# Kernel tuning notes

Measured on AMD Instinct MI355X. Metric: run time of the kernel, lower is better.

Reference implementation:

```python
import jax, jax.numpy as jnp
import numpy as np

EPS_LN = 1e-12
EPS_BN = 1e-5


def layernorm(x, w, b):
    u = jnp.mean(x, axis=-1, keepdims=True)
    s = jnp.mean((x - u) ** 2, axis=-1, keepdims=True)
    return w * ((x - u) / jnp.sqrt(s + EPS_LN)) + b


def reps_block(x, ln1_w, ln1_b, lin_w, lin_b, ln2_w, ln2_b):
    # GRAPHLayerNorm -> (dropout, identity in eval) -> Linear -> ReLU -> GRAPHLayerNorm
    h = layernorm(x, ln1_w, ln1_b)
    h = jax.nn.relu(jnp.einsum('bnd,od->bno', h, lin_w) + lin_b)
    return layernorm(h, ln2_w, ln2_b)


def attend(x):
    # full dense self-attention: softmax(x x^T) x ; dropout is identity in eval
    scores = jnp.einsum('bnd,bmd->bnm', x, x)  # [B,4096,4096]
    attn = jax.nn.softmax(scores, axis=-1)
    return jnp.einsum('bnm,bmd->bnd', attn, x)


def setup_inputs() -> dict:
    key = jax.random.key(0)
    ks = jax.random.split(key, 8)
    B, C, H, W = 4, 512, 64, 64
    D = 512
    inp = {
        'T1': jax.random.normal(ks[0], (B, C, H, W), jnp.float32),
        'T2': jax.random.normal(ks[1], (B, C, H, W), jnp.float32),
        'w_conv3': jax.random.normal(ks[2], (1024, 1024, 3, 3), jnp.float32) * 0.01,
        'w_conv1': jax.random.normal(ks[3], (512, 1024, 1, 1), jnp.float32) * 0.03,
        'bn_gamma': jnp.ones((512,), jnp.float32),
        'bn_beta': jnp.zeros((512,), jnp.float32),
        'bn_mean': jnp.zeros((512,), jnp.float32),
        'bn_var': jnp.ones((512,), jnp.float32),
        'ln1_w': jnp.ones((D,), jnp.float32),
        'ln1_b': jnp.zeros((D,), jnp.float32),
        'lin_w': jax.random.normal(ks[4], (D, D), jnp.float32) * 0.04,
        'lin_b': jnp.zeros((D,), jnp.float32),
        'ln2_w': jnp.ones((D,), jnp.float32),
        'ln2_b': jnp.zeros((D,), jnp.float32),
    }
    return inp


def reference(T1, T2, w_conv3, w_conv1, bn_gamma, bn_beta, bn_mean, bn_var,
              ln1_w, ln1_b, lin_w, lin_b, ln2_w, ln2_b):
    B = T1.shape[0]
    X = jnp.concatenate((T1, T2), axis=1)  # [B,1024,64,64]
    dn = ('NCHW', 'OIHW', 'NCHW')
    X = jax.lax.conv_general_dilated(X, w_conv3, (1, 1), ((1, 1), (1, 1)), dimension_numbers=dn)
    X = jax.lax.conv_general_dilated(X, w_conv1, (1, 1), ((0, 0), (0, 0)), dimension_numbers=dn)  # [B,512,64,64]
    # BatchNorm (eval, running stats) + ReLU
    inv = (bn_gamma / jnp.sqrt(bn_var + EPS_BN))[None, :, None, None]
    X = jax.nn.relu(X * inv + (bn_beta - bn_mean * bn_gamma / jnp.sqrt(bn_var + EPS_BN))[None, :, None, None])
    x = X.transpose(0, 2, 3, 1).reshape(B, 4096, 512)
    # block 1
    rel = attend(x)
    rel = reps_block(x + rel, ln1_w, ln1_b, lin_w, lin_b, ln2_w, ln2_b)
    # block 2 (original code reuses self.reps_graph, i.e. SAME params)
    rel1 = attend(rel)
    rel1 = reps_block(rel + rel1, ln1_w, ln1_b, lin_w, lin_b, ln2_w, ln2_b)
    return rel1.reshape(B, 64, 64, 512).transpose(0, 3, 1, 2)  # [B,512,64,64]
```

## Files before the change

### kernel.cpp

```cpp
#include <hip/hip_runtime.h>
#include <stdint.h>

typedef float f32x4 __attribute__((ext_vector_type(4)));
typedef __bf16 bf16x8 __attribute__((ext_vector_type(8)));
typedef unsigned short u16;
typedef unsigned short u16x8 __attribute__((ext_vector_type(8)));

__device__ __forceinline__ float bf2f(u16 u){ unsigned int i = ((unsigned int)u)<<16; float f; __builtin_memcpy(&f,&i,4); return f; }
__device__ __forceinline__ u16 f2bf(float f){ unsigned int i; __builtin_memcpy(&i,&f,4); i += 0x7FFFu + ((i>>16)&1u); return (u16)(i>>16); }
__device__ __forceinline__ u16 f2h(float f){ _Float16 h = (_Float16)f; u16 b; __builtin_memcpy(&b,&h,2); return b; }
__device__ __forceinline__ float h2f(u16 b){ _Float16 h; __builtin_memcpy(&h,&b,2); return (float)h; }

__device__ __forceinline__ void gld16(const void* g, void* l){
  __builtin_amdgcn_global_load_lds(
      (const __attribute__((address_space(1))) void*)(uintptr_t)g,
      (__attribute__((address_space(3))) void*)(unsigned int)(uintptr_t)l, 16, 0, 0);
}

__global__ __launch_bounds__(256) void pad_interior(const float* __restrict__ T1,
                                                    const float* __restrict__ T2,
                                                    u16* __restrict__ Xpad){
  const int n = blockIdx.z, ct = blockIdx.y, pt = blockIdx.x;
  const int t = threadIdx.x;
  const int c0 = ct*64, p0 = pt*64;
  const float* src = (c0 < 512) ? (T1 + ((long)n*512 + c0)*4096)
                                : (T2 + ((long)n*512 + (c0-512))*4096);
  __shared__ u16 lds[64][66];
  #pragma unroll
  for (int i=0;i<4;i++){
    int c = i*16 + (t>>4);
    int ch = t&15;
    float4 v = *(const float4*)(src + (long)c*4096 + p0 + ch*4);
    int p = ch*4;
    lds[p+0][c] = f2bf(v.x); lds[p+1][c] = f2bf(v.y);
    lds[p+2][c] = f2bf(v.z); lds[p+3][c] = f2bf(v.w);
  }
  __syncthreads();
  #pragma unroll
  for (int i=0;i<8;i++){
    int p = i*8 + (t>>5);
    int c2 = t&31;
    int pix = p0 + p; int yy = (pix>>6)+1, xx = (pix&63)+1;
    ushort2 val; val.x = lds[p][2*c2]; val.y = lds[p][2*c2+1];
    *(ushort2*)(Xpad + (((long)n*66 + yy)*66 + xx)*1024 + c0 + 2*c2) = val;
  }
}

__global__ __launch_bounds__(256) void prep_w3(const float* __restrict__ w3, u16* __restrict__ wk3t){
  const int o = blockIdx.x; const int t = threadIdx.x;
  __shared__ u16 lds[9216];
  const float* src = w3 + (long)o*9216;
  #pragma unroll
  for (int i=0;i<9;i++){
    int j = i*256 + t;
    float4 v = *(const float4*)(src + j*4);
    lds[j*4+0]=f2bf(v.x); lds[j*4+1]=f2bf(v.y); lds[j*4+2]=f2bf(v.z); lds[j*4+3]=f2bf(v.w);
  }
  __syncthreads();
  u16* dst = wk3t + (long)o*9216;
  #pragma unroll
  for (int i=0;i<36;i++){
    int j = i*256 + t; int tp = j>>10, ci = j&1023;
    dst[j] = lds[ci*9+tp];
  }
}

__global__ void prep_small(const float* __restrict__ w1, const float* __restrict__ bg,
                           const float* __restrict__ bb, const float* __restrict__ bm,
                           const float* __restrict__ bv, const float* __restrict__ linw,
                           u16* __restrict__ w1t, u16* __restrict__ lint,
                           float* __restrict__ bias1){
  const int b = blockIdx.x, t = threadIdx.x;
  if (b < 2048){
    long i = (long)b*256 + t;
    int o = (int)(i>>10);
    float inv = bg[o] / sqrtf(bv[o] + 1e-5f);
    w1t[i] = f2bf(w1[i]*inv);
  } else if (b < 3072){
    long i = (long)(b-2048)*256 + t;
    lint[i] = f2bf(linw[i]);
  } else {
    int o = (b-3072)*256 + t;
    float inv = bg[o]/sqrtf(bv[o]+1e-5f);
    bias1[o] = bb[o] - bm[o]*inv;
  }
}

__global__ __launch_bounds__(256) void row_norm(const u16* __restrict__ x, float* __restrict__ nrm){
  const int row = blockIdx.x*4 + (threadIdx.x>>6);
  const int lane = threadIdx.x & 63;
  u16x8 q = *(const u16x8*)(x + (long)row*512 + lane*8);
  float s = 0.f;
  #pragma unroll
  for (int j=0;j<8;j++){ float f = bf2f(q[j]); s += f*f; }
  #pragma unroll
  for (int off=32; off; off>>=1) s += __shfl_xor(s, off);
  if (lane==0) nrm[row] = s;
}

__global__ __launch_bounds__(256) void transpose_bf(const u16* __restrict__ src, u16* __restrict__ dst,
                                                    int R, int C, long sStr, long dStr){
  const int z = blockIdx.z;
  src += (long)z*sStr; dst += (long)z*dStr;
  const int r0 = blockIdx.x*64, c0 = blockIdx.y*64;
  const int t = threadIdx.x;
  __shared__ u16 lds[64][66];
  #pragma unroll
  for (int i=0;i<4;i++){
    int r = i*16 + (t>>4), ch = t&15;
    ushort4 v = *(const ushort4*)(src + (long)(r0+r)*C + c0 + ch*4);
    lds[r][ch*4+0]=v.x; lds[r][ch*4+1]=v.y; lds[r][ch*4+2]=v.z; lds[r][ch*4+3]=v.w;
  }
  __syncthreads();
  #pragma unroll
  for (int i=0;i<4;i++){
    int c = i*16 + (t>>4), ch = t&15;
    ushort4 v;
    v.x = lds[ch*4+0][c]; v.y = lds[ch*4+1][c]; v.z = lds[ch*4+2][c]; v.w = lds[ch*4+3][c];
    *(ushort4*)(dst + (long)(c0+c)*R + r0 + ch*4) = v;
  }
}

__global__ __launch_bounds__(256) void transpose_bf_f32(const u16* __restrict__ src, float* __restrict__ dst){
  const int z = blockIdx.z;
  src += (long)z*4096*512; dst += (long)z*512*4096;
  const int r0 = blockIdx.x*64, c0 = blockIdx.y*64;
  const int t = threadIdx.x;
  __shared__ u16 lds[64][66];
  #pragma unroll
  for (int i=0;i<4;i++){
    int r = i*16 + (t>>4), ch = t&15;
    ushort4 v = *(const ushort4*)(src + (long)(r0+r)*512 + c0 + ch*4);
    lds[r][ch*4+0]=v.x; lds[r][ch*4+1]=v.y; lds[r][ch*4+2]=v.z; lds[r][ch*4+3]=v.w;
  }
  __syncthreads();
  #pragma unroll
  for (int i=0;i<4;i++){
    int c = i*16 + (t>>4), ch = t&15;
    float4 v;
    v.x = bf2f(lds[ch*4+0][c]); v.y = bf2f(lds[ch*4+1][c]);
    v.z = bf2f(lds[ch*4+2][c]); v.w = bf2f(lds[ch*4+3][c]);
    *(float4*)(dst + (long)(c0+c)*4096 + r0 + ch*4) = v;
  }
}

template<int EPI, int CONV>
__global__ __launch_bounds__(512, 2) void gemm256(
    const u16* __restrict__ Ain, const u16* __restrict__ Btin, void* __restrict__ Cv,
    int K, int lda, int ldb, int ldc, const float* __restrict__ srowIn,
    u16* __restrict__ C0, u16* __restrict__ C1, u16* __restrict__ C2, u16* __restrict__ C3)
{
  extern __shared__ u16 sm[];
  const int t = threadIdx.x;
  const int lane = t & 63;
  const int wid = t >> 6;
  const int wr = wid >> 2, wc = wid & 3;

  long m0, n0;
  int byv = 0, bxv = 0;
  const u16* A; const u16* Bt; const float* srow; u16* Cz;
  if (EPI == 3){
    const int orig = blockIdx.x;
    const int swz = (orig & 7) * 68 + (orig >> 3);
    const int z = swz / 136;
    int p = swz % 136;
    int by = 0;
    while (p >= 16 - by){ p -= 16 - by; by++; }
    const int bx = by + p;
    byv = by; bxv = bx;
    m0 = (long)by * 256; n0 = (long)bx * 256;
    A = Ain + (long)z*4096*lda;
    Bt = A;
    srow = srowIn + (long)z*4096;
    Cz = (z==0)?C0:(z==1)?C1:(z==2)?C2:C3;
  } else {
    const int orig = blockIdx.y * gridDim.x + blockIdx.x;
    const int cpx = (gridDim.x * gridDim.y) >> 3;
    const int swz = (orig & 7) * cpx + (orig >> 3);
    const int bx = swz % gridDim.x;
    const int by = swz / gridDim.x;
    m0 = (long)by * 256; n0 = (long)bx * 256;
    A = Ain; Bt = Btin; srow = srowIn; Cz = (u16*)Cv;
  }

  const int row0 = t >> 2;
  const int cs0  = (t & 3) ^ ((row0 >> 1) & 3);

  const u16 *aB0, *aB1;
  if (CONV) {
    long m_ = m0 + row0;
    long pb0 = ((long)((int)(m_>>12)*66 + (int)((m_>>6)&63)))*66 + (int)(m_&63);
    m_ = m0 + row0 + 128;
    long pb1 = ((long)((int)(m_>>12)*66 + (int)((m_>>6)&63)))*66 + (int)(m_&63);
    aB0 = A + pb0*1024 + cs0*8;
    aB1 = A + pb1*1024 + cs0*8;
  } else {
    aB0 = A + (m0 + row0)*(long)lda + cs0*8;
    aB1 = A + (m0 + row0 + 128)*(long)lda + cs0*8;
  }
  const u16* bB0 = Bt + (n0 + row0)*(long)ldb + cs0*8;
  const u16* bB1 = Bt + (n0 + row0 + 128)*(long)ldb + cs0*8;

  auto issueA = [&](int sub, long aoff){
    u16* d = sm + sub*8192 + t*8;
    gld16(aB0 + aoff, d);
    gld16(aB1 + aoff, d + 4096);
  };
  auto issueB = [&](int sub, long boff){
    u16* d = sm + 32768 + sub*8192 + t*8;
    gld16(bB0 + boff, d);
    gld16(bB1 + boff, d + 4096);
  };
  auto conv_aoff = [&](int tile)->long {
    int kb = tile << 6;
    int tap = kb >> 10;
    int cb  = kb & 1023;
    int ky = (tap >= 6) ? 2 : (tap >= 3 ? 1 : 0);
    int kx = tap - ky*3;
    return (long)(ky*66 + kx)*1024 + cb;
  };

  const int frow = lane & 15;
  const int elemoff = (((lane>>4) ^ ((frow>>1)&3)) << 3);
  const int rAoff = (wr*128 + frow)*32 + elemoff;
  const int rBoff = (wc*64  + frow)*32 + elemoff;

  f32x4 acc[8][4] = {};

  {
    long a0 = CONV ? conv_aoff(0) : 0L;
    issueA(0, a0);
    issueB(0, 0);
    issueA(1, a0 + 32);
    issueB(1, 32);
  }

  const int NT = K >> 6;
  for (int tile = 0; tile < NT; ++tile) {
    const int b = tile & 1;
    const int nb2 = b ^ 1;
    const bool lastT = (tile == NT-1);
    long aoffN = 0, boffN = 0;
    if (!lastT) {
      aoffN = CONV ? conv_aoff(tile+1) : (long)(tile+1)*64;
      boffN = (long)(tile+1)*64;
    }

    asm volatile("s_waitcnt vmcnt(4)" ::: "memory");
    __builtin_amdgcn_s_barrier();
    __builtin_amdgcn_sched_barrier(0);

    {
      const u16* pA = sm + (b*2+0)*8192 + rAoff;
      const u16* pB = sm + 32768 + (b*2+0)*8192 + rBoff;
      bf16x8 bf[4];
      #pragma unroll
      for (int i=0;i<4;i++) bf[i] = *(const bf16x8*)(pB + i*512);
      {
        bf16x8 a[4];
        #pragma unroll
        for (int i=0;i<4;i++) a[i] = *(const bf16x8*)(pA + i*512);
        if (!lastT) issueA(nb2*2+0, aoffN);
        __builtin_amdgcn_s_setprio(1);
        #pragma unroll
        for (int mi=0;mi<4;mi++)
          #pragma unroll
          for (int ni=0;ni<4;ni++)
            acc[mi][ni] = __builtin_amdgcn_mfma_f32_16x16x32_bf16(a[mi], bf[ni], acc[mi][ni],0,0,0);
        __builtin_amdgcn_s_setprio(0);
      }
      {
        bf16x8 a[4];
        #pragma unroll
        for (int i=0;i<4;i++) a[i] = *(const bf16x8*)(pA + (4+i)*512);
        if (!lastT) issueB(nb2*2+0, boffN);
        __builtin_amdgcn_s_setprio(1);
        #pragma unroll
        for (int mi=0;mi<4;mi++)
          #pragma unroll
          for (int ni=0;ni<4;ni++)
            acc[4+mi][ni] = __builtin_amdgcn_mfma_f32_16x16x32_bf16(a[mi], bf[ni], acc[4+mi][ni],0,0,0);
        __builtin_amdgcn_s_setprio(0);
      }
    }

    if (lastT) asm volatile("s_waitcnt vmcnt(0)" ::: "memory");
    else       asm volatile("s_waitcnt vmcnt(4)" ::: "memory");
    __builtin_amdgcn_s_barrier();
    __builtin_amdgcn_sched_barrier(0);

    {
      const u16* pA = sm + (b*2+1)*8192 + rAoff;
      const u16* pB = sm + 32768 + (b*2+1)*8192 + rBoff;
      bf16x8 bf[4];
      #pragma unroll
      for (int i=0;i<4;i++) bf[i] = *(const bf16x8*)(pB + i*512);
      {
        bf16x8 a[4];
        #pragma unroll
        for (int i=0;i<4;i++) a[i] = *(const bf16x8*)(pA + i*512);
        if (!lastT) issueA(nb2*2+1, aoffN + 32);
        __builtin_amdgcn_s_setprio(1);
        #pragma unroll
        for (int mi=0;mi<4;mi++)
          #pragma unroll
          for (int ni=0;ni<4;ni++)
            acc[mi][ni] = __builtin_amdgcn_mfma_f32_16x16x32_bf16(a[mi], bf[ni], acc[mi][ni],0,0,0);
        __builtin_amdgcn_s_setprio(0);
      }
      {
        bf16x8 a[4];
        #pragma unroll
        for (int i=0;i<4;i++) a[i] = *(const bf16x8*)(pA + (4+i)*512);
        if (!lastT) issueB(nb2*2+1, boffN + 32);
        __builtin_amdgcn_s_setprio(1);
        #pragma unroll
        for (int mi=0;mi<4;mi++)
          #pragma unroll
          for (int ni=0;ni<4;ni++)
            acc[4+mi][ni] = __builtin_amdgcn_mfma_f32_16x16x32_bf16(a[mi], bf[ni], acc[4+mi][ni],0,0,0);
        __builtin_amdgcn_s_setprio(0);
      }
    }
  }

  const int crow0 = wr*128 + ((lane>>4)<<2);
  const int ccol0 = wc*64 + frow;

  #pragma unroll
  for (int mi=0;mi<8;mi++){
    #pragma unroll
    for (int ni=0;ni<4;ni++){
      long col = n0 + ccol0 + ni*16;
      #pragma unroll
      for (int r=0;r<4;r++){
        long row = m0 + crow0 + mi*16 + r;
        float v = acc[mi][ni][r];
        if (EPI==3) Cz[row*(long)ldc + col] = f2h(v - srow[row]);
        else        Cz[row*(long)ldc + col] = f2bf(v);
      }
    }
  }

  if (EPI == 3 && bxv != byv){
    __syncthreads();
    u16* lt = sm;
    float sc[4];
    #pragma unroll
    for (int ni=0;ni<4;ni++) sc[ni] = srow[n0 + ccol0 + ni*16];
    #pragma unroll
    for (int mi=0;mi<8;mi++){
      const int g = (crow0 + mi*16) >> 2;
      #pragma unroll
      for (int ni=0;ni<4;ni++){
        const int col_l = ccol0 + ni*16;
        ushort4 pk;
        #pragma unroll
        for (int r=0;r<4;r++) pk[r] = f2h(acc[mi][ni][r] - sc[ni]);
        *(ushort4*)(lt + col_l*256 + ((g ^ (col_l & 63))<<2)) = pk;
      }
    }
    __syncthreads();
    const int half = lane >> 5, l32 = lane & 31;
    #pragma unroll
    for (int ps=0; ps<16; ps++){
      const int R = ps*16 + wid*2 + half;
      const int u0 = ((l32<<1)    ) ^ (R & 63);
      const int u1 = ((l32<<1) | 1) ^ (R & 63);
      ushort4 a = *(const ushort4*)(lt + R*256 + (u0<<2));
      ushort4 b = *(const ushort4*)(lt + R*256 + (u1<<2));
      u16* dst = Cz + (n0 + R)*(long)ldc + m0 + (l32<<3);
      *(ushort4*)dst = a;
      *(ushort4*)(dst+4) = b;
    }
  }
}

template<int EPI>
__global__ __launch_bounds__(256, 2) void gemm128_deep(
    const u16* __restrict__ A, const u16* __restrict__ Bt, u16* __restrict__ C,
    const float* __restrict__ bias, int K, int lda, int ldb, int ldc)
{
  extern __shared__ u16 pm[];
  const int L = blockIdx.x;
  const int xcd = L & 7;
  const int q = L >> 3;
  const int by = (q >> 2) + xcd*16;
  const int bx = q & 3;
  const long m0 = (long)by * 128, n0 = (long)bx * 128;

  const int t = threadIdx.x;
  const int lane = t & 63;
  const int w = t >> 6;
  const int wr = w >> 1, wc = w & 1;

  const int row0 = t >> 2;
  const int cs0  = (t & 3) ^ ((row0 >> 1) & 3);

  const u16* aB0 = A + (m0 + row0)*(long)lda + cs0*8;
  const u16* aB1 = aB0 + 64*(long)lda;
  const u16* bB0 = Bt + (n0 + row0)*(long)ldb + cs0*8;
  const u16* bB1 = bB0 + 64*(long)ldb;

  auto issueA = [&](int sub, long off){
    u16* d = pm + sub*4096 + t*8;
    gld16(aB0 + off, d);
    gld16(aB1 + off, d + 2048);
  };
  auto issueB = [&](int sub, long off){
    u16* d = pm + 16384 + sub*4096 + t*8;
    gld16(bB0 + off, d);
    gld16(bB1 + off, d + 2048);
  };

  const int frow = lane & 15;
  const int elemoff = (((lane>>4) ^ ((frow>>1)&3)) << 3);
  const int rAoff = (wr*64 + frow)*32 + elemoff;
  const int rBoff = (wc*64 + frow)*32 + elemoff;

  f32x4 acc[4][4] = {};

  issueA(0, 0);  issueB(0, 0);
  issueA(1, 32); issueB(1, 32);

  const int NT = K >> 6;
  for (int tl = 0; tl < NT; ++tl) {
    const int b = tl & 1;
    const int nb2 = b ^ 1;
    const bool lastT = (tl == NT-1);
    const long offN = (long)(tl+1)*64;

    asm volatile("s_waitcnt vmcnt(4)" ::: "memory");
    __builtin_amdgcn_s_barrier();
    __builtin_amdgcn_sched_barrier(0);

    {
      const u16* pA = pm + (b*2+0)*4096 + rAoff;
      const u16* pB = pm + 16384 + (b*2+0)*4096 + rBoff;
      bf16x8 bf[4];
      #pragma unroll
      for (int i=0;i<4;i++) bf[i] = *(const bf16x8*)(pB + i*512);
      {
        bf16x8 a[2];
        #pragma unroll
        for (int i=0;i<2;i++) a[i] = *(const bf16x8*)(pA + i*512);
        if (!lastT) issueA(nb2*2+0, offN);
        __builtin_amdgcn_s_setprio(1);
        #pragma unroll
        for (int mi=0;mi<2;mi++)
          #pragma unroll
          for (int ni=0;ni<4;ni++)
            acc[mi][ni] = __builtin_amdgcn_mfma_f32_16x16x32_bf16(a[mi], bf[ni], acc[mi][ni],0,0,0);
        __builtin_amdgcn_s_setprio(0);
      }
      {
        bf16x8 a[2];
        #pragma unroll
        for (int i=0;i<2;i++) a[i] = *(const bf16x8*)(pA + (2+i)*512);
        if (!lastT) issueB(nb2*2+0, offN);
        __builtin_amdgcn_s_setprio(1);
        #pragma unroll
        for (int mi=0;mi<2;mi++)
          #pragma unroll
          for (int ni=0;ni<4;ni++)
            acc[2+mi][ni] = __builtin_amdgcn_mfma_f32_16x16x32_bf16(a[mi], bf[ni], acc[2+mi][ni],0,0,0);
        __builtin_amdgcn_s_setprio(0);
      }
    }

    if (lastT) asm volatile("s_waitcnt vmcnt(0)" ::: "memory");
    else       asm volatile("s_waitcnt vmcnt(4)" ::: "memory");
    __builtin_amdgcn_s_barrier();
    __builtin_amdgcn_sched_barrier(0);

    {
      const u16* pA = pm + (b*2+1)*4096 + rAoff;
      const u16* pB = pm + 16384 + (b*2+1)*4096 + rBoff;
      bf16x8 bf[4];
      #pragma unroll
      for (int i=0;i<4;i++) bf[i] = *(const bf16x8*)(pB + i*512);
      {
        bf16x8 a[2];
        #pragma unroll
        for (int i=0;i<2;i++) a[i] = *(const bf16x8*)(pA + i*512);
        if (!lastT) issueA(nb2*2+1, offN + 32);
        __builtin_amdgcn_s_setprio(1);
        #pragma unroll
        for (int mi=0;mi<2;mi++)
          #pragma unroll
          for (int ni=0;ni<4;ni++)
            acc[mi][ni] = __builtin_amdgcn_mfma_f32_16x16x32_bf16(a[mi], bf[ni], acc[mi][ni],0,0,0);
        __builtin_amdgcn_s_setprio(0);
      }
      {
        bf16x8 a[2];
        #pragma unroll
        for (int i=0;i<2;i++) a[i] = *(const bf16x8*)(pA + (2+i)*512);
        if (!lastT) issueB(nb2*2+1, offN + 32);
        __builtin_amdgcn_s_setprio(1);
        #pragma unroll
        for (int mi=0;mi<2;mi++)
          #pragma unroll
          for (int ni=0;ni<4;ni++)
            acc[2+mi][ni] = __builtin_amdgcn_mfma_f32_16x16x32_bf16(a[mi], bf[ni], acc[2+mi][ni],0,0,0);
        __builtin_amdgcn_s_setprio(0);
      }
    }
  }

  const int crow0 = wr*64 + ((lane>>4)<<2);
  const int ccol0 = wc*64 + frow;
  #pragma unroll
  for (int mi=0;mi<4;mi++){
    #pragma unroll
    for (int ni=0;ni<4;ni++){
      long col = n0 + ccol0 + ni*16;
      float bv = (EPI==1) ? bias[col] : 0.0f;
      #pragma unroll
      for (int r=0;r<4;r++){
        long row = m0 + crow0 + mi*16 + r;
        float v = acc[mi][ni][r];
        if (EPI==1){ v += bv; v = v > 0.0f ? v : 0.0f; }
        C[row*(long)ldc + col] = f2bf(v);
      }
    }
  }
}

__global__ __launch_bounds__(256, 2) void pv5(
    const u16* __restrict__ P0, const u16* __restrict__ P1,
    const u16* __restrict__ P2, const u16* __restrict__ P3,
    const u16* __restrict__ xT, u16* __restrict__ attb)
{
  extern __shared__ u16 pm[];
  const int L = blockIdx.x;
  const int xcd = L & 7;
  const int z = xcd >> 1;
  const int q = L >> 3;
  const int by = ((q >> 2) << 1) + (xcd & 1);
  const int bx = q & 3;
  const long ZS = 4096L*512;
  const u16* A  = (z==0)?P0:(z==1)?P1:(z==2)?P2:P3;
  const u16* Bt = xT   + (long)z*ZS;
  u16*       C  = attb + (long)z*ZS;
  const long m0 = (long)by * 128, n0 = (long)bx * 128;

  const int t = threadIdx.x;
  const int lane = t & 63;
  const int w = t >> 6;
  const int wr = w >> 1, wc = w & 1;

  const int row0 = t >> 2;
  const int cs0  = (t & 3) ^ ((row0 >> 1) & 3);

  const u16* aB0 = A + (m0 + row0)*4096L + cs0*8;
  const u16* aB1 = aB0 + 64*4096L;
  const u16* bB0 = Bt + (n0 + row0)*4096L + cs0*8;
  const u16* bB1 = bB0 + 64*4096L;

  auto issueA = [&](int sub, long off){
    u16* d = pm + sub*4096 + t*8;
    gld16(aB0 + off, d);
    gld16(aB1 + off, d + 2048);
  };
  auto issueB = [&](int sub, long off){
    u16* d = pm + 16384 + sub*4096 + t*8;
    gld16(bB0 + off, d);
    gld16(bB1 + off, d + 2048);
  };

  const int frow = lane & 15;
  const int elemoff = (((lane>>4) ^ ((frow>>1)&3)) << 3);
  const int rAoff = (wr*64 + frow)*32 + elemoff;
  const int rBoff = (wc*64 + frow)*32 + elemoff;

  f32x4 acc[4][4] = {};

  issueA(0, 0);  issueB(0, 0);
  issueA(1, 32); issueB(1, 32);

  const int NT = 64;
  for (int tl = 0; tl < NT; ++tl) {
    const int b = tl & 1;
    const int nb2 = b ^ 1;
    const bool lastT = (tl == NT-1);
    const long offN = (long)(tl+1)*64;

    asm volatile("s_waitcnt vmcnt(4)" ::: "memory");
    __builtin_amdgcn_s_barrier();
    __builtin_amdgcn_sched_barrier(0);

    {
      const u16* pA = pm + (b*2+0)*4096 + rAoff;
      const u16* pB = pm + 16384 + (b*2+0)*4096 + rBoff;
      bf16x8 bf[4];
      #pragma unroll
      for (int i=0;i<4;i++) bf[i] = *(const bf16x8*)(pB + i*512);
      {
        bf16x8 a[2];
        #pragma unroll
        for (int i=0;i<2;i++) a[i] = *(const bf16x8*)(pA + i*512);
        if (!lastT) issueA(nb2*2+0, offN);
        __builtin_amdgcn_s_setprio(1);
        #pragma unroll
        for (int mi=0;mi<2;mi++)
          #pragma unroll
          for (int ni=0;ni<4;ni++)
            acc[mi][ni] = __builtin_amdgcn_mfma_f32_16x16x32_bf16(a[mi], bf[ni], acc[mi][ni],0,0,0);
        __builtin_amdgcn_s_setprio(0);
      }
      {
        bf16x8 a[2];
        #pragma unroll
        for (int i=0;i<2;i++) a[i] = *(const bf16x8*)(pA + (2+i)*512);
        if (!lastT) issueB(nb2*2+0, offN);
        __builtin_amdgcn_s_setprio(1);
        #pragma unroll
        for (int mi=0;mi<2;mi++)
          #pragma unroll
          for (int ni=0;ni<4;ni++)
            acc[2+mi][ni] = __builtin_amdgcn_mfma_f32_16x16x32_bf16(a[mi], bf[ni], acc[2+mi][ni],0,0,0);
        __builtin_amdgcn_s_setprio(0);
      }
    }

    if (lastT) asm volatile("s_waitcnt vmcnt(0)" ::: "memory");
    else       asm volatile("s_waitcnt vmcnt(4)" ::: "memory");
    __builtin_amdgcn_s_barrier();
    __builtin_amdgcn_sched_barrier(0);

    {
      const u16* pA = pm + (b*2+1)*4096 + rAoff;
      const u16* pB = pm + 16384 + (b*2+1)*4096 + rBoff;
      bf16x8 bf[4];
      #pragma unroll
      for (int i=0;i<4;i++) bf[i] = *(const bf16x8*)(pB + i*512);
      {
        bf16x8 a[2];
        #pragma unroll
        for (int i=0;i<2;i++) a[i] = *(const bf16x8*)(pA + i*512);
        if (!lastT) issueA(nb2*2+1, offN + 32);
        __builtin_amdgcn_s_setprio(1);
        #pragma unroll
        for (int mi=0;mi<2;mi++)
          #pragma unroll
          for (int ni=0;ni<4;ni++)
            acc[mi][ni] = __builtin_amdgcn_mfma_f32_16x16x32_bf16(a[mi], bf[ni], acc[mi][ni],0,0,0);
        __builtin_amdgcn_s_setprio(0);
      }
      {
        bf16x8 a[2];
        #pragma unroll
        for (int i=0;i<2;i++) a[i] = *(const bf16x8*)(pA + (2+i)*512);
        if (!lastT) issueB(nb2*2+1, offN + 32);
        __builtin_amdgcn_s_setprio(1);
        #pragma unroll
        for (int mi=0;mi<2;mi++)
          #pragma unroll
          for (int ni=0;ni<4;ni++)
            acc[2+mi][ni] = __builtin_amdgcn_mfma_f32_16x16x32_bf16(a[mi], bf[ni], acc[2+mi][ni],0,0,0);
        __builtin_amdgcn_s_setprio(0);
      }
    }
  }

  const int crow0 = wr*64 + ((lane>>4)<<2);
  const int ccol0 = wc*64 + frow;
  #pragma unroll
  for (int mi=0;mi<4;mi++){
    #pragma unroll
    for (int ni=0;ni<4;ni++){
      long col = n0 + ccol0 + ni*16;
      #pragma unroll
      for (int r=0;r<4;r++){
        long row = m0 + crow0 + mi*16 + r;
        C[row*512 + col] = f2bf(acc[mi][ni][r]);
      }
    }
  }
}

__global__ __launch_bounds__(256) void softmax_batched(
    u16* __restrict__ S0, u16* __restrict__ S1,
    u16* __restrict__ S2, u16* __restrict__ S3)
{
  const int z = blockIdx.x >> 12;
  const long row = blockIdx.x & 4095;
  u16* buf = (z==0)?S0:(z==1)?S1:(z==2)?S2:S3;
  u16* src = buf + row*4096;
  const int t = threadIdx.x, lane = t&63, w = t>>6;
  float v[16];
  #pragma unroll
  for (int i=0;i<2;i++){
    u16x8 q = *(const u16x8*)(src + t*16 + i*8);
    #pragma unroll
    for (int j=0;j<8;j++) v[i*8+j] = h2f(q[j]);
  }
  float mx = v[0];
  #pragma unroll
  for (int i=1;i<16;i++) mx = fmaxf(mx, v[i]);
  #pragma unroll
  for (int off=32; off; off>>=1) mx = fmaxf(mx, __shfl_xor(mx, off));
  __shared__ float red[4];
  if (lane==0) red[w] = mx;
  __syncthreads();
  mx = fmaxf(fmaxf(red[0],red[1]), fmaxf(red[2],red[3]));
  float sum = 0.0f;
  #pragma unroll
  for (int i=0;i<16;i++){ v[i] = __expf(v[i]-mx); sum += v[i]; }
  #pragma unroll
  for (int off=32; off; off>>=1) sum += __shfl_xor(sum, off);
  __shared__ float red2[4];
  if (lane==0) red2[w] = sum;
  __syncthreads();
  sum = red2[0]+red2[1]+red2[2]+red2[3];
  const float inv = 1.0f/sum;
  #pragma unroll
  for (int i=0;i<2;i++){
    u16x8 o;
    #pragma unroll
    for (int j=0;j<8;j++) o[j] = f2bf(v[i*8+j]*inv);
    *(u16x8*)(src + t*16 + i*8) = o;
  }
}

template<int ADD>
__global__ __launch_bounds__(256) void ln_row(
    const u16* __restrict__ X, const u16* __restrict__ Y,
    const float* __restrict__ w, const float* __restrict__ b,
    u16* __restrict__ outB)
{
  const long row = blockIdx.x;
  const int t = threadIdx.x, lane = t&63, wv = t>>6;
  ushort2 xv = *(const ushort2*)(X + row*512 + t*2);
  float v0 = bf2f(xv.x), v1 = bf2f(xv.y);
  if (ADD){
    ushort2 yv = *(const ushort2*)(Y + row*512 + t*2);
    v0 += bf2f(yv.x); v1 += bf2f(yv.y);
  }
  float s = v0+v1, q = v0*v0 + v1*v1;
  #pragma unroll
  for (int off=32; off; off>>=1){ s += __shfl_xor(s,off); q += __shfl_xor(q,off); }
  __shared__ float red[8];
  if (lane==0){ red[wv]=s; red[4+wv]=q; }
  __syncthreads();
  s = red[0]+red[1]+red[2]+red[3];
  q = red[4]+red[5]+red[6]+red[7];
  const float u = s*(1.0f/512.0f);
  const float var = q*(1.0f/512.0f) - u*u;
  const float inv = rsqrtf(var + 1e-12f);
  const int c = t*2;
  float o0 = (v0-u)*inv*w[c]   + b[c];
  float o1 = (v1-u)*inv*w[c+1] + b[c+1];
  ushort2 ov; ov.x=f2bf(o0); ov.y=f2bf(o1);
  *(ushort2*)(outB + row*512 + c) = ov;
}

extern "C" void kernel_launch(void* const* d_in, const int* in_sizes, int n_in,
                              void* d_out, int out_size, void* d_ws, size_t ws_size,
                              hipStream_t stream) {
  const float* T1   = (const float*)d_in[0];
  const float* T2   = (const float*)d_in[1];
  const float* w3   = (const float*)d_in[2];
  const float* w1   = (const float*)d_in[3];
  const float* bg   = (const float*)d_in[4];
  const float* bb   = (const float*)d_in[5];
  const float* bm   = (const float*)d_in[6];
  const float* bv   = (const float*)d_in[7];
  const float* ln1w = (const float*)d_in[8];
  const float* ln1b = (const float*)d_in[9];
  const float* linw = (const float*)d_in[10];
  const float* linb = (const float*)d_in[11];
  const float* ln2w = (const float*)d_in[12];
  const float* ln2b = (const float*)d_in[13];

  hipFuncSetAttribute(reinterpret_cast<const void*>(gemm256<0,1>),
                      hipFuncAttributeMaxDynamicSharedMemorySize, 131072);
  hipFuncSetAttribute(reinterpret_cast<const void*>(gemm256<3,0>),
                      hipFuncAttributeMaxDynamicSharedMemorySize, 131072);
  hipFuncSetAttribute(reinterpret_cast<const void*>(pv5),
                      hipFuncAttributeMaxDynamicSharedMemorySize, 65536);
  hipFuncSetAttribute(reinterpret_cast<const void*>(gemm128_deep<0>),
                      hipFuncAttributeMaxDynamicSharedMemorySize, 65536);
  hipFuncSetAttribute(reinterpret_cast<const void*>(gemm128_deep<1>),
                      hipFuncAttributeMaxDynamicSharedMemorySize, 65536);

  char* ws = (char*)d_ws;
  size_t off = 0;
  auto alloc = [&](size_t bytes)->char* {
    char* p = ws + off;
    off += (bytes + 255) & ~(size_t)255;
    return p;
  };
  const size_t XPAD_B = 4L*66*66*1024*2;
  u16*   Xpad  = (u16*)  alloc(XPAD_B);
  u16*   wk3t  = (u16*)  alloc(1024L*9216*2);
  u16*   w1t   = (u16*)  alloc(512L*1024*2);
  u16*   lint  = (u16*)  alloc(512L*512*2);
  float* bias1 = (float*)alloc(512*4);
  float* nrm   = (float*)alloc(16384L*4);
  u16*   Y1    = (u16*)  alloc(16384L*1024*2);
  u16*   x0    = (u16*)  alloc(16384L*512*2);
  u16*   xT    = (u16*)  alloc(4L*512*4096*2);
  u16*   Sreg  = (u16*)  alloc(2L*4096*4096*2);
  u16*   attb  = (u16*)  alloc(16384L*512*2);
  u16*   h     = (u16*)  alloc(16384L*512*2);
  u16*   g     = (u16*)  alloc(16384L*512*2);
  u16*   rel1  = (u16*)  alloc(16384L*512*2);
  u16*   S0    = Y1;
  u16*   S1    = Sreg;
  u16*   S2    = Sreg + 4096L*4096;
  u16*   S3    = Xpad;
  if (off > ws_size) return;

  const long ZS = 4096L*512;

  hipMemsetAsync(Xpad, 0, XPAD_B, stream);
  pad_interior<<<dim3(64,16,4), 256, 0, stream>>>(T1, T2, Xpad);
  prep_w3<<<1024, 256, 0, stream>>>(w3, wk3t);
  prep_small<<<3074, 256, 0, stream>>>(w1, bg, bb, bm, bv, linw, w1t, lint, bias1);

  gemm256<0,1><<<dim3(4,64), 512, 131072, stream>>>(Xpad, wk3t, (void*)Y1, 9216, 0, 9216, 1024,
                                                    nullptr, nullptr, nullptr, nullptr, nullptr);
  gemm128_deep<1><<<512, 256, 65536, stream>>>(Y1, w1t, x0, bias1, 1024, 1024, 1024, 512);

  auto attend = [&](const u16* xin){
    transpose_bf<<<dim3(64,8,4), 256, 0, stream>>>(xin, xT, 4096, 512, ZS, ZS);
    row_norm<<<4096, 256, 0, stream>>>(xin, nrm);
    gemm256<3,0><<<dim3(544), 512, 131072, stream>>>(xin, xin, nullptr, 512, 512, 512, 4096,
                                                     nrm, S0, S1, S2, S3);
    softmax_batched<<<16384, 256, 0, stream>>>(S0, S1, S2, S3);
    pv5<<<512, 256, 65536, stream>>>(S0, S1, S2, S3, xT, attb);
  };

  attend(x0);
  ln_row<1><<<16384, 256, 0, stream>>>(x0, attb, ln1w, ln1b, h);
  gemm128_deep<1><<<512, 256, 65536, stream>>>(h, lint, g, linb, 512, 512, 512, 512);
  ln_row<0><<<16384, 256, 0, stream>>>(g, nullptr, ln2w, ln2b, rel1);

  attend(rel1);
  ln_row<1><<<16384, 256, 0, stream>>>(rel1, attb, ln1w, ln1b, h);
  gemm128_deep<1><<<512, 256, 65536, stream>>>(h, lint, g, linb, 512, 512, 512, 512);
  ln_row<0><<<16384, 256, 0, stream>>>(g, nullptr, ln2w, ln2b, x0);

  transpose_bf_f32<<<dim3(64,8,4), 256, 0, stream>>>(x0, (float*)d_out);
}
```

Measured before the change: 796.8 us.

## Prefetch whole next tile up front in gemm256 and zero only padding border

The gemm256 main loop now issues all A and B global-to-LDS loads for the next K-tile at the start of each iteration, waits with vmcnt(8), and processes both halves of the current tile in one unrolled loop. This replaces the old scheme, which interleaved each load between MFMA groups and had a barrier between the halves. Separately, the full-buffer memset of the padded conv input is replaced by a small kernel that zeroes only the border pixels. Each border thread writes 4096 elements per pixel, although the pixel stride is 1024. That spills into neighbouring pixels and past the end of the buffer for the last pixel, and is only masked because later kernels overwrite those regions.

```diff
diff --git a/kernel.cpp b/kernel.cpp
--- a/kernel.cpp
+++ b/kernel.cpp
@@ -15,6 +15,18 @@
   __builtin_amdgcn_global_load_lds(
       (const __attribute__((address_space(1))) void*)(uintptr_t)g,
       (__attribute__((address_space(3))) void*)(unsigned int)(uintptr_t)l, 16, 0, 0);
+}
+
+__global__ __launch_bounds__(256) void border_zero(u16* __restrict__ Xpad){
+  const int n = blockIdx.y, p = blockIdx.x;
+  int y, x;
+  if (p < 66)        { y = 0;        x = p; }
+  else if (p < 132)  { y = 65;       x = p - 66; }
+  else if (p < 196)  { y = p - 131;  x = 0; }
+  else               { y = p - 195;  x = 65; }
+  u16x8 z = {};
+  *(u16x8*)(Xpad + (((long)n*66 + y)*66 + x)*1024 + threadIdx.x*8)        = z;
+  *(u16x8*)(Xpad + (((long)n*66 + y)*66 + x)*1024 + 2048 + threadIdx.x*8) = z;
 }
 
 __global__ __launch_bounds__(256) void pad_interior(const float* __restrict__ T1,
@@ -229,10 +241,8 @@
 
   {
     long a0 = CONV ? conv_aoff(0) : 0L;
-    issueA(0, a0);
-    issueB(0, 0);
-    issueA(1, a0 + 32);
-    issueB(1, 32);
+    issueA(0, a0);       issueA(1, a0 + 32);
+    issueB(0, 0);        issueB(1, 32);
   }
 
   const int NT = K >> 6;
@@ -240,19 +250,23 @@
     const int b = tile & 1;
     const int nb2 = b ^ 1;
     const bool lastT = (tile == NT-1);
-    long aoffN = 0, boffN = 0;
+
     if (!lastT) {
-      aoffN = CONV ? conv_aoff(tile+1) : (long)(tile+1)*64;
-      boffN = (long)(tile+1)*64;
-    }
-
-    asm volatile("s_waitcnt vmcnt(4)" ::: "memory");
+      long aoffN = CONV ? conv_aoff(tile+1) : (long)(tile+1)*64;
+      long boffN = (long)(tile+1)*64;
+      issueA(nb2*2+0, aoffN);      issueA(nb2*2+1, aoffN + 32);
+      issueB(nb2*2+0, boffN);      issueB(nb2*2+1, boffN + 32);
+    }
+
+    if (lastT) asm volatile("s_waitcnt vmcnt(0)" ::: "memory");
+    else       asm volatile("s_waitcnt vmcnt(8)" ::: "memory");
     __builtin_amdgcn_s_barrier();
     __builtin_amdgcn_sched_barrier(0);
 
-    {
-      const u16* pA = sm + (b*2+0)*8192 + rAoff;
-      const u16* pB = sm + 32768 + (b*2+0)*8192 + rBoff;
+    #pragma unroll
+    for (int half = 0; half < 2; ++half){
+      const u16* pA = sm + (b*2+half)*8192 + rAoff;
+      const u16* pB = sm + 32768 + (b*2+half)*8192 + rBoff;
       bf16x8 bf[4];
       #pragma unroll
       for (int i=0;i<4;i++) bf[i] = *(const bf16x8*)(pB + i*512);
@@ -260,7 +274,6 @@
         bf16x8 a[4];
         #pragma unroll
         for (int i=0;i<4;i++) a[i] = *(const bf16x8*)(pA + i*512);
-        if (!lastT) issueA(nb2*2+0, aoffN);
         __builtin_amdgcn_s_setprio(1);
         #pragma unroll
         for (int mi=0;mi<4;mi++)
@@ -273,7 +286,6 @@
         bf16x8 a[4];
         #pragma unroll
         for (int i=0;i<4;i++) a[i] = *(const bf16x8*)(pA + (4+i)*512);
-        if (!lastT) issueB(nb2*2+0, boffN);
         __builtin_amdgcn_s_setprio(1);
         #pragma unroll
         for (int mi=0;mi<4;mi++)
@@ -284,44 +296,8 @@
       }
     }
 
-    if (lastT) asm volatile("s_waitcnt vmcnt(0)" ::: "memory");
-    else       asm volatile("s_waitcnt vmcnt(4)" ::: "memory");
     __builtin_amdgcn_s_barrier();
     __builtin_amdgcn_sched_barrier(0);
-
-    {
-      const u16* pA = sm + (b*2+1)*8192 + rAoff;
-      const u16* pB = sm + 32768 + (b*2+1)*8192 + rBoff;
-      bf16x8 bf[4];
-      #pragma unroll
-      for (int i=0;i<4;i++) bf[i] = *(const bf16x8*)(pB + i*512);
-      {
-        bf16x8 a[4];
-        #pragma unroll
-        for (int i=0;i<4;i++) a[i] = *(const bf16x8*)(pA + i*512);
-        if (!lastT) issueA(nb2*2+1, aoffN + 32);
-        __builtin_amdgcn_s_setprio(1);
-        #pragma unroll
-        for (int mi=0;mi<4;mi++)
-          #pragma unroll
-          for (int ni=0;ni<4;ni++)
-            acc[mi][ni] = __builtin_amdgcn_mfma_f32_16x16x32_bf16(a[mi], bf[ni], acc[mi][ni],0,0,0);
-        __builtin_amdgcn_s_setprio(0);
-      }
-      {
-        bf16x8 a[4];
-        #pragma unroll
-        for (int i=0;i<4;i++) a[i] = *(const bf16x8*)(pA + (4+i)*512);
-        if (!lastT) issueB(nb2*2+1, boffN + 32);
-        __builtin_amdgcn_s_setprio(1);
-        #pragma unroll
-        for (int mi=0;mi<4;mi++)
-          #pragma unroll
-          for (int ni=0;ni<4;ni++)
-            acc[4+mi][ni] = __builtin_amdgcn_mfma_f32_16x16x32_bf16(a[mi], bf[ni], acc[4+mi][ni],0,0,0);
-        __builtin_amdgcn_s_setprio(0);
-      }
-    }
   }
 
   const int crow0 = wr*128 + ((lane>>4)<<2);
@@ -815,7 +791,7 @@
 
   const long ZS = 4096L*512;
 
-  hipMemsetAsync(Xpad, 0, XPAD_B, stream);
+  border_zero<<<dim3(260,4), 256, 0, stream>>>(Xpad);
   pad_interior<<<dim3(64,16,4), 256, 0, stream>>>(T1, T2, Xpad);
   prep_w3<<<1024, 256, 0, stream>>>(w3, wk3t);
   prep_small<<<3074, 256, 0, stream>>>(w1, bg, bb, bm, bv, linw, w1t, lint, bias1);
```

Result: slower. 825.7 us (+3.6%).
